# Kernel tuning notes

Measured on AMD Instinct MI355X. Metric: run time of the kernel, lower is better.

The kernel has to match this reference:

```python
import jax, jax.numpy as jnp
import numpy as np

E = 768       # embed dim
NH = 12       # heads
HD = 64       # head dim
WIN = 14      # window size
DEPTH = 12
PATCH = 16
WINDOW_IDX = (0, 1, 3, 4, 6, 7, 9, 10)
EPS = 1e-6


def layer_norm(x, w, b):
    mu = jnp.mean(x, axis=-1, keepdims=True)
    var = jnp.mean(jnp.square(x - mu), axis=-1, keepdims=True)
    return (x - mu) * jax.lax.rsqrt(var + EPS) * w + b


def get_rel_pos(size, rel_pos):
    # q_size == k_size -> direct lookup, no interpolation
    coords = jnp.arange(size)
    rel = coords[:, None] - coords[None, :] + (size - 1)
    return rel_pos[rel]  # (size, size, HD)


def attention(x, qkv_w, qkv_b, proj_w, proj_b, rel_h, rel_w):
    B, H, W, _ = x.shape
    N = H * W
    qkv = (x.reshape(B, N, E) @ qkv_w + qkv_b).reshape(B, N, 3, NH, HD)
    q = qkv[:, :, 0].transpose(0, 2, 1, 3).reshape(B * NH, N, HD)
    k = qkv[:, :, 1].transpose(0, 2, 1, 3).reshape(B * NH, N, HD)
    v = qkv[:, :, 2].transpose(0, 2, 1, 3).reshape(B * NH, N, HD)
    attn = (q * (HD ** -0.5)) @ k.transpose(0, 2, 1)  # (B*NH, N, N)
    # decomposed relative position bias
    Rh = get_rel_pos(H, rel_h)  # (H, H, HD)
    Rw = get_rel_pos(W, rel_w)  # (W, W, HD)
    r_q = q.reshape(B * NH, H, W, HD)
    rh = jnp.einsum('bhwc,hkc->bhwk', r_q, Rh)
    rw = jnp.einsum('bhwc,wkc->bhwk', r_q, Rw)
    attn = attn.reshape(B * NH, H, W, H, W) + rh[:, :, :, :, None] + rw[:, :, :, None, :]
    attn = jax.nn.softmax(attn.reshape(B * NH, N, N), axis=-1)
    out = (attn @ v).reshape(B, NH, H, W, HD).transpose(0, 2, 3, 1, 4).reshape(B, H, W, E)
    return out @ proj_w + proj_b


def window_partition(x, ws):
    B, H, W, C = x.shape
    pad_h, pad_w = (-H) % ws, (-W) % ws
    x = jnp.pad(x, ((0, 0), (0, pad_h), (0, pad_w), (0, 0)))
    Hp, Wp = H + pad_h, W + pad_w
    x = x.reshape(B, Hp // ws, ws, Wp // ws, ws, C).transpose(0, 1, 3, 2, 4, 5)
    return x.reshape(-1, ws, ws, C), (Hp, Wp)


def window_unpartition(win, ws, pad_hw, hw):
    Hp, Wp = pad_hw
    H, W = hw
    B = win.shape[0] // ((Hp // ws) * (Wp // ws))
    x = win.reshape(B, Hp // ws, Wp // ws, ws, ws, -1).transpose(0, 1, 3, 2, 4, 5)
    return x.reshape(B, Hp, Wp, -1)[:, :H, :W]


def _forward(x, patch_w, patch_b, pos_embed,
             ln1_w, ln1_b, qkv_w, qkv_b, proj_w, proj_b,
             rel_h_win, rel_w_win, rel_h_glob, rel_w_glob,
             ln2_w, ln2_b, fc1_w, fc1_b, fc2_w, fc2_b, out_w, out_b):
    # patch embed: conv 16x16 stride 16
    x = jax.lax.conv_general_dilated(
        x, patch_w, (PATCH, PATCH), 'VALID',
        dimension_numbers=('NCHW', 'OIHW', 'NCHW'))
    x = x.transpose(0, 2, 3, 1) + patch_b  # (B, H, W, C)
    x = x + pos_embed
    win_i, glob_i = 0, 0
    for i in range(DEPTH):
        shortcut = x
        h = layer_norm(x, ln1_w[i], ln1_b[i])
        if i in WINDOW_IDX:
            hw = h.shape[1:3]
            h, pad_hw = window_partition(h, WIN)
            h = attention(h, qkv_w[i], qkv_b[i], proj_w[i], proj_b[i],
                          rel_h_win[win_i], rel_w_win[win_i])
            h = window_unpartition(h, WIN, pad_hw, hw)
            win_i += 1
        else:
            h = attention(h, qkv_w[i], qkv_b[i], proj_w[i], proj_b[i],
                          rel_h_glob[glob_i], rel_w_glob[glob_i])
            glob_i += 1
        x = shortcut + h
        h = layer_norm(x, ln2_w[i], ln2_b[i])
        h = jax.nn.gelu(h @ fc1_w[i] + fc1_b[i], approximate=False) @ fc2_w[i] + fc2_b[i]
        x = x + h
    feat = x.transpose(0, 3, 1, 2)  # (B, C, H, W) == 'last_feat'
    return jnp.einsum('bchw,oc->bohw', feat, out_w) + out_b[None, :, None, None]


def setup_inputs() -> dict:
    key = jax.random.key(0)
    ks = iter(jax.random.split(key, 64))
    def n(shape, s=0.02):
        return jax.random.normal(next(ks), shape, jnp.float32) * s
    B, IMG = 2, 512
    G = IMG // PATCH  # 32
    return {
        'x': jax.random.normal(next(ks), (B, 3, IMG, IMG), jnp.float32),
        'patch_w': n((E, 3, PATCH, PATCH)),
        'patch_b': jnp.zeros((E,), jnp.float32),
        'pos_embed': n((1, G, G, E)),
        'ln1_w': jnp.ones((DEPTH, E), jnp.float32),
        'ln1_b': jnp.zeros((DEPTH, E), jnp.float32),
        'qkv_w': n((DEPTH, E, 3 * E)),
        'qkv_b': jnp.zeros((DEPTH, 3 * E), jnp.float32),
        'proj_w': n((DEPTH, E, E)),
        'proj_b': jnp.zeros((DEPTH, E), jnp.float32),
        'rel_h_win': n((8, 2 * WIN - 1, HD)),
        'rel_w_win': n((8, 2 * WIN - 1, HD)),
        'rel_h_glob': n((4, 2 * G - 1, HD)),
        'rel_w_glob': n((4, 2 * G - 1, HD)),
        'ln2_w': jnp.ones((DEPTH, E), jnp.float32),
        'ln2_b': jnp.zeros((DEPTH, E), jnp.float32),
        'fc1_w': n((DEPTH, E, 4 * E)),
        'fc1_b': jnp.zeros((DEPTH, 4 * E), jnp.float32),
        'fc2_w': n((DEPTH, 4 * E, E)),
        'fc2_b': jnp.zeros((DEPTH, E), jnp.float32),
        'out_w': n((256, E)),
        'out_b': jnp.zeros((256,), jnp.float32),
    }


def reference(x, patch_w, patch_b, pos_embed,
              ln1_w, ln1_b, qkv_w, qkv_b, proj_w, proj_b,
              rel_h_win, rel_w_win, rel_h_glob, rel_w_glob,
              ln2_w, ln2_b, fc1_w, fc1_b, fc2_w, fc2_b, out_w, out_b):
    return _forward(x, patch_w, patch_b, pos_embed,
                    ln1_w, ln1_b, qkv_w, qkv_b, proj_w, proj_b,
                    rel_h_win, rel_w_win, rel_h_glob, rel_w_glob,
                    ln2_w, ln2_b, fc1_w, fc1_b, fc2_w, fc2_b, out_w, out_b)
```

## Files before the change

### kernel.cpp

```cpp
#include <hip/hip_runtime.h>
#include <hip/hip_bf16.h>
#include <math.h>

static constexpr int E   = 768;
static constexpr int NH  = 12;
static constexpr int HD  = 64;
static constexpr int Bsz = 2;
static constexpr int G   = 32;
static constexpr int NTOK = G * G;
static constexpr int ROWS = Bsz * NTOK;
static constexpr int WS  = 14;
static constexpr int NWIN_SIDE = 3;
static constexpr int NWIN = NWIN_SIDE * NWIN_SIDE;
static constexpr int BW  = Bsz * NWIN;
static constexpr int NW  = WS * WS;
static constexpr int WROWS = BW * NW;
static constexpr int WIN_MASK = 0x6DB;

typedef __attribute__((ext_vector_type(8))) short short8;
typedef __attribute__((ext_vector_type(4))) float f32x4;
typedef unsigned short ushort_t;

__device__ __forceinline__ unsigned short f2bf(float x) {
  union { float f; unsigned u; } v; v.f = x;
  unsigned r = v.u + 0x7fffu + ((v.u >> 16) & 1u);
  return (unsigned short)(r >> 16);
}
__device__ __forceinline__ float bf2f(unsigned short h) {
  union { unsigned u; float f; } v; v.u = ((unsigned)h) << 16;
  return v.f;
}

__device__ __forceinline__ void glds16(const void* g, void* l) {
  __builtin_amdgcn_global_load_lds(
      (const __attribute__((address_space(1))) unsigned*)g,
      (__attribute__((address_space(3))) unsigned*)l, 16, 0, 0);
}

__global__ __launch_bounds__(256) void ln_kernel(
    const float* __restrict__ in, const float* __restrict__ w,
    const float* __restrict__ b, ushort_t* __restrict__ out) {
  const int wave = threadIdx.x >> 6, lane = threadIdx.x & 63;
  const int row = blockIdx.x * 4 + wave;
  const float4* r4 = (const float4*)(in + (size_t)row * E);
  float4 v[3];
  v[0] = r4[lane]; v[1] = r4[lane + 64]; v[2] = r4[lane + 128];
  float s = 0.f, s2 = 0.f;
#pragma unroll
  for (int i = 0; i < 3; i++) {
    s += v[i].x + v[i].y + v[i].z + v[i].w;
    s2 += v[i].x * v[i].x + v[i].y * v[i].y + v[i].z * v[i].z + v[i].w * v[i].w;
  }
#pragma unroll
  for (int off = 1; off <= 32; off <<= 1) {
    s += __shfl_xor(s, off);
    s2 += __shfl_xor(s2, off);
  }
  const float mean = s * (1.f / E);
  const float var  = s2 * (1.f / E) - mean * mean;
  const float rs   = rsqrtf(var + 1e-6f);
  ushort_t* o = out + (size_t)row * E;
#pragma unroll
  for (int i = 0; i < 3; i++) {
    const int e0 = (lane + i * 64) * 4;
    ushort4 p;
    p.x = f2bf((v[i].x - mean) * rs * w[e0]     + b[e0]);
    p.y = f2bf((v[i].y - mean) * rs * w[e0 + 1] + b[e0 + 1]);
    p.z = f2bf((v[i].z - mean) * rs * w[e0 + 2] + b[e0 + 2]);
    p.w = f2bf((v[i].w - mean) * rs * w[e0 + 3] + b[e0 + 3]);
    *(ushort4*)&o[e0] = p;
  }
}

enum { OP_QKV = 0, OP_GELU = 1, OP_ADD = 2, OP_POS = 3, OP_HEAD = 4 };

template <int OP, int MAP>
__global__ __launch_bounds__(256) void gemm_bt(
    const ushort_t* __restrict__ A, const ushort_t* __restrict__ Bt,
    const float* __restrict__ bias, const float* __restrict__ res,
    const float* __restrict__ pos, void* __restrict__ Cp,
    int M, int N, int K, int ncol) {
  __shared__ ushort_t As[2][64 * 64];
  __shared__ ushort_t Bs[2][64 * 64];
  const int tid = threadIdx.x, wave = tid >> 6, lane = tid & 63;
  const int lx = lane & 15, ly = lane >> 4;

  const int nwg = gridDim.x;
  const int q = nwg >> 3, r = nwg & 7;
  const int xcd = blockIdx.x & 7, loc = blockIdx.x >> 3;
  const int wgid = ((xcd < r) ? xcd * (q + 1) : r * (q + 1) + (xcd - r) * q) + loc;
  const int brow = wgid / ncol, bcol = wgid - brow * ncol;
  const int row0 = brow * 64, col0 = bcol * 64;
  const int wm = (wave >> 1) * 32, wn = (wave & 1) * 32;
  const int rin = lane >> 3, pseg = lane & 7;
  const int lseg = pseg ^ rin;
  f32x4 acc[2][2] = {};

  const ushort_t* aptr[2];
  const ushort_t* bptr[2];
#pragma unroll
  for (int j = 0; j < 2; j++) {
    const int slot = wave * 2 + j;
    int ar = row0 + slot * 8 + rin;
    if (ar >= M) ar = M - 1;
    if (MAP == 2) {
      const int bI = ar >> 10, t = ar & 1023, y = t >> 5, x = t & 31;
      const int by = y / WS, wy = y - by * WS;
      const int bx = x / WS, wx = x - bx * WS;
      const int win = bI * NWIN + by * NWIN_SIDE + bx;
      aptr[j] = &A[((size_t)win * NW + wy * WS + wx) * E + lseg * 8];
    } else {
      aptr[j] = &A[(size_t)ar * K + lseg * 8];
    }
    const int br = col0 + slot * 8 + rin;
    bptr[j] = &Bt[(size_t)br * K + lseg * 8];
  }

#pragma unroll
  for (int j = 0; j < 2; j++) {
    const int slot = wave * 2 + j;
    glds16(aptr[j], &As[0][slot * 512]);
    glds16(bptr[j], &Bs[0][slot * 512]);
  }

  const int nt = K >> 6;
  for (int t = 0; t < nt; t++) {
    const int cur = t & 1;
    if (t + 1 < nt) {
      const int k1 = (t + 1) << 6;
#pragma unroll
      for (int j = 0; j < 2; j++) {
        const int slot = wave * 2 + j;
        glds16(aptr[j] + k1, &As[cur ^ 1][slot * 512]);
        glds16(bptr[j] + k1, &Bs[cur ^ 1][slot * 512]);
      }
      asm volatile("s_waitcnt vmcnt(4)" ::: "memory");
    } else {
      asm volatile("s_waitcnt vmcnt(0)" ::: "memory");
    }
    __builtin_amdgcn_s_barrier();
    __builtin_amdgcn_sched_barrier(0);
#pragma unroll
    for (int kb = 0; kb < 2; kb++) {
      short8 af[2], bfm[2];
#pragma unroll
      for (int m = 0; m < 2; m++) {
        const int rr = wm + m * 16 + lx;
        af[m] = *(const short8*)&As[cur][rr * 64 + (((kb * 4 + ly) ^ (rr & 7)) * 8)];
      }
#pragma unroll
      for (int n = 0; n < 2; n++) {
        const int rr = wn + n * 16 + lx;
        bfm[n] = *(const short8*)&Bs[cur][rr * 64 + (((kb * 4 + ly) ^ (rr & 7)) * 8)];
      }
      __builtin_amdgcn_s_setprio(1);
#pragma unroll
      for (int m = 0; m < 2; m++)
#pragma unroll
        for (int n = 0; n < 2; n++)
          acc[m][n] = __builtin_amdgcn_mfma_f32_16x16x32_bf16(af[m], bfm[n], acc[m][n], 0, 0, 0);
      __builtin_amdgcn_s_setprio(0);
    }
    asm volatile("s_waitcnt lgkmcnt(0)" ::: "memory");
    __builtin_amdgcn_s_barrier();
    __builtin_amdgcn_sched_barrier(0);
  }

#pragma unroll
  for (int m = 0; m < 2; m++) {
#pragma unroll
    for (int r4 = 0; r4 < 4; r4++) {
      const int gr = row0 + wm + m * 16 + ly * 4 + r4;
      if (gr >= M) continue;
#pragma unroll
      for (int n = 0; n < 2; n++) {
        const int gc = col0 + wn + n * 16 + lx;
        float v = acc[m][n][r4] + bias[gc];
        if (OP == OP_GELU) v = 0.5f * v * (1.f + erff(v * 0.70710678118654752f));
        if (OP == OP_ADD)  v += res[(size_t)gr * N + gc];
        if (OP == OP_POS)  v += pos[(size_t)(gr & 1023) * N + gc];
        if (OP == OP_QKV || OP == OP_GELU)
          ((ushort_t*)Cp)[(size_t)gr * N + gc] = f2bf(v);
        else if (OP == OP_HEAD)
          ((float*)Cp)[(((size_t)(gr >> 10) * 256 + gc) << 10) | (gr & 1023)] = v;
        else
          ((float*)Cp)[(size_t)gr * N + gc] = v;
      }
    }
  }
}

template <int OP, int MAP>
__global__ __launch_bounds__(128) void gemm_32(
    const ushort_t* __restrict__ A, const ushort_t* __restrict__ Bt,
    const float* __restrict__ bias, const float* __restrict__ res,
    const float* __restrict__ pos, void* __restrict__ Cp,
    int M, int N, int K, int ncol) {
  __shared__ ushort_t As[2][32 * 64];
  __shared__ ushort_t Bs[2][64 * 64];
  const int tid = threadIdx.x, wave = tid >> 6, lane = tid & 63;
  const int lx = lane & 15, ly = lane >> 4;

  const int nwg = gridDim.x;
  const int q = nwg >> 3, r = nwg & 7;
  const int xcd = blockIdx.x & 7, loc = blockIdx.x >> 3;
  const int wgid = ((xcd < r) ? xcd * (q + 1) : r * (q + 1) + (xcd - r) * q) + loc;
  const int brow = wgid / ncol, bcol = wgid - brow * ncol;
  const int row0 = brow * 32, col0 = bcol * 64;
  const int wn = wave * 32;
  const int rin = lane >> 3, pseg = lane & 7;
  const int lseg = pseg ^ rin;
  f32x4 acc[2][2] = {};

  const ushort_t* aptr[2];
  const ushort_t* bptr[4];
#pragma unroll
  for (int j = 0; j < 2; j++) {
    const int slot = wave * 2 + j;
    int ar = row0 + slot * 8 + rin;
    if (ar >= M) ar = M - 1;
    if (MAP == 2) {
      const int bI = ar >> 10, t = ar & 1023, y = t >> 5, x = t & 31;
      const int by = y / WS, wy = y - by * WS;
      const int bx = x / WS, wx = x - bx * WS;
      const int win = bI * NWIN + by * NWIN_SIDE + bx;
      aptr[j] = &A[((size_t)win * NW + wy * WS + wx) * E + lseg * 8];
    } else {
      aptr[j] = &A[(size_t)ar * K + lseg * 8];
    }
  }
#pragma unroll
  for (int j = 0; j < 4; j++) {
    const int slot = wave * 4 + j;
    const int br = col0 + slot * 8 + rin;
    bptr[j] = &Bt[(size_t)br * K + lseg * 8];
  }

#pragma unroll
  for (int j = 0; j < 2; j++) glds16(aptr[j], &As[0][(wave * 2 + j) * 512]);
#pragma unroll
  for (int j = 0; j < 4; j++) glds16(bptr[j], &Bs[0][(wave * 4 + j) * 512]);

  const int nt = K >> 6;
  for (int t = 0; t < nt; t++) {
    const int cur = t & 1;
    if (t + 1 < nt) {
      const int k1 = (t + 1) << 6;
#pragma unroll
      for (int j = 0; j < 2; j++) glds16(aptr[j] + k1, &As[cur ^ 1][(wave * 2 + j) * 512]);
#pragma unroll
      for (int j = 0; j < 4; j++) glds16(bptr[j] + k1, &Bs[cur ^ 1][(wave * 4 + j) * 512]);
      asm volatile("s_waitcnt vmcnt(6)" ::: "memory");
    } else {
      asm volatile("s_waitcnt vmcnt(0)" ::: "memory");
    }
    __builtin_amdgcn_s_barrier();
    __builtin_amdgcn_sched_barrier(0);
#pragma unroll
    for (int kb = 0; kb < 2; kb++) {
      short8 af[2], bfm[2];
#pragma unroll
      for (int m = 0; m < 2; m++) {
        const int rr = m * 16 + lx;
        af[m] = *(const short8*)&As[cur][rr * 64 + (((kb * 4 + ly) ^ (rr & 7)) * 8)];
      }
#pragma unroll
      for (int n = 0; n < 2; n++) {
        const int rr = wn + n * 16 + lx;
        bfm[n] = *(const short8*)&Bs[cur][rr * 64 + (((kb * 4 + ly) ^ (rr & 7)) * 8)];
      }
      __builtin_amdgcn_s_setprio(1);
#pragma unroll
      for (int m = 0; m < 2; m++)
#pragma unroll
        for (int n = 0; n < 2; n++)
          acc[m][n] = __builtin_amdgcn_mfma_f32_16x16x32_bf16(af[m], bfm[n], acc[m][n], 0, 0, 0);
      __builtin_amdgcn_s_setprio(0);
    }
    asm volatile("s_waitcnt lgkmcnt(0)" ::: "memory");
    __builtin_amdgcn_s_barrier();
    __builtin_amdgcn_sched_barrier(0);
  }

#pragma unroll
  for (int m = 0; m < 2; m++) {
#pragma unroll
    for (int r4 = 0; r4 < 4; r4++) {
      const int gr = row0 + m * 16 + ly * 4 + r4;
      if (gr >= M) continue;
#pragma unroll
      for (int n = 0; n < 2; n++) {
        const int gc = col0 + wn + n * 16 + lx;
        float v = acc[m][n][r4] + bias[gc];
        if (OP == OP_GELU) v = 0.5f * v * (1.f + erff(v * 0.70710678118654752f));
        if (OP == OP_ADD)  v += res[(size_t)gr * N + gc];
        if (OP == OP_POS)  v += pos[(size_t)(gr & 1023) * N + gc];
        if (OP == OP_QKV || OP == OP_GELU)
          ((ushort_t*)Cp)[(size_t)gr * N + gc] = f2bf(v);
        else if (OP == OP_HEAD)
          ((float*)Cp)[(((size_t)(gr >> 10) * 256 + gc) << 10) | (gr & 1023)] = v;
        else
          ((float*)Cp)[(size_t)gr * N + gc] = v;
      }
    }
  }
}

__global__ __launch_bounds__(128) void attn_mfma(
    const ushort_t* __restrict__ qkv, ushort_t* __restrict__ out,
    const float* __restrict__ relh, const float* __restrict__ relw,
    int Hd, int Wd) {
  const int Ntok = Hd * Wd;
  __shared__ ushort_t smem[11392];
  ushort_t* Ks   = smem;
  ushort_t* Vst  = smem + 2048;
  ushort_t* Ps   = smem + 4608;
  ushort_t* Qs   = smem;
  ushort_t* RelS = smem + 2048;
  ushort_t* Th   = smem + 6144;
  ushort_t* Tw   = smem + 8256;
  ushort_t* khw  = smem + 10368;

  const int tid = threadIdx.x, wave = tid >> 6, lane = tid & 63;
  const int lx = lane & 15, ly = lane >> 4;
  const int bh = blockIdx.y, b = bh / NH, nh = bh % NH;
  const int q0 = blockIdx.x * 32;
  const size_t base = (size_t)b * Ntok * 2304 + nh * 64;

#pragma unroll
  for (int i = 0; i < 2; i++) {
    const int fv = i * 128 + tid;
    const int row = fv >> 3, dv8 = (fv & 7) * 8;
    const int qq = min(q0 + row, Ntok - 1);
    short8 v = *(const short8*)&qkv[base + (size_t)qq * 2304 + dv8];
    *(short8*)&Qs[(row * 64 + dv8) ^ ((row & 7) << 3)] = v;
  }
  for (int k = tid; k < 1024; k += 128) {
    const int kc = min(k, Ntok - 1);
    const int kh = kc / Wd;
    khw[k] = (ushort_t)((kh << 8) | (kc - kh * Wd));
  }
  __syncthreads();

  short8 qa[2];
  {
    const int row = wave * 16 + lx;
#pragma unroll
    for (int kb = 0; kb < 2; kb++)
      qa[kb] = *(const short8*)&Qs[(row * 64 + kb * 32 + ly * 8) ^ ((row & 7) << 3)];
  }
  int qh_r[4], qw_r[4];
#pragma unroll
  for (int r = 0; r < 4; r++) {
    const int qc = min(q0 + wave * 16 + ly * 4 + r, Ntok - 1);
    qh_r[r] = qc / Wd;
    qw_r[r] = qc - qh_r[r] * Wd;
  }

  for (int t = 0; t < 2; t++) {
    const float* rel = t ? relw : relh;
    const int TR = t ? (2 * Wd - 1) : (2 * Hd - 1);
    __syncthreads();
#pragma unroll
    for (int i = 0; i < 4; i++) {
      const int fv = i * 128 + tid;
      const int row = fv >> 3, c8 = (fv & 7) * 8;
      short8 v = {};
      if (row < TR) {
        const float* rp = &rel[(size_t)row * 64 + c8];
        const float4 a = *(const float4*)rp;
        const float4 bq = *(const float4*)(rp + 4);
        v[0] = (short)f2bf(a.x);  v[1] = (short)f2bf(a.y);
        v[2] = (short)f2bf(a.z);  v[3] = (short)f2bf(a.w);
        v[4] = (short)f2bf(bq.x); v[5] = (short)f2bf(bq.y);
        v[6] = (short)f2bf(bq.z); v[7] = (short)f2bf(bq.w);
      }
      *(short8*)&RelS[(row * 64 + c8) ^ ((row & 7) << 3)] = v;
    }
    __syncthreads();
    const int NT = (TR + 15) >> 4;
    ushort_t* T = t ? Tw : Th;
    for (int nt = 0; nt < NT; nt++) {
      f32x4 a = {};
      __builtin_amdgcn_s_setprio(1);
#pragma unroll
      for (int kb = 0; kb < 2; kb++) {
        const int rrow = nt * 16 + lx;
        short8 bfv = *(const short8*)&RelS[(rrow * 64 + kb * 32 + ly * 8) ^ ((rrow & 7) << 3)];
        a = __builtin_amdgcn_mfma_f32_16x16x32_bf16(qa[kb], bfv, a, 0, 0, 0);
      }
      __builtin_amdgcn_s_setprio(0);
#pragma unroll
      for (int reg = 0; reg < 4; reg++)
        T[(wave * 16 + ly * 4 + reg) * 66 + nt * 16 + lx] = f2bf(a[reg]);
    }
  }

  f32x4 o[4] = {};
  float m_[4], l_[4];
#pragma unroll
  for (int r = 0; r < 4; r++) { m_[r] = -3e38f; l_[r] = 0.f; }

  const int nkt = (Ntok + 31) >> 5;
  const int srow = tid >> 3, c7 = tid & 7, dv8s = c7 * 8;
  const int vswz = (c7 & 3) << 3;

  short8 kpre[2], vpre[2];
#pragma unroll
  for (int i = 0; i < 2; i++) {
    const int gk = srow + i * 16;
    short8 kv = {}, vv = {};
    if (gk < Ntok) {
      kv = *(const short8*)&qkv[base + 768 + (size_t)gk * 2304 + dv8s];
      vv = *(const short8*)&qkv[base + 1536 + (size_t)gk * 2304 + dv8s];
    }
    kpre[i] = kv; vpre[i] = vv;
  }

  for (int kt = 0; kt < nkt; kt++) {
    __syncthreads();
#pragma unroll
    for (int i = 0; i < 2; i++) {
      const int row = srow + i * 16;
      *(short8*)&Ks[(row * 64 + dv8s) ^ ((row & 7) << 3)] = kpre[i];
      const int kcol = row ^ vswz;
#pragma unroll
      for (int j = 0; j < 8; j++)
        Vst[(dv8s + j) * 40 + kcol] = (ushort_t)vpre[i][j];
    }
    if (kt + 1 < nkt) {
#pragma unroll
      for (int i = 0; i < 2; i++) {
        const int gk = (kt + 1) * 32 + srow + i * 16;
        short8 kv = {}, vv = {};
        if (gk < Ntok) {
          kv = *(const short8*)&qkv[base + 768 + (size_t)gk * 2304 + dv8s];
          vv = *(const short8*)&qkv[base + 1536 + (size_t)gk * 2304 + dv8s];
        }
        kpre[i] = kv; vpre[i] = vv;
      }
    }
    __syncthreads();

    f32x4 c[2] = {};
    __builtin_amdgcn_s_setprio(1);
#pragma unroll
    for (int kb = 0; kb < 2; kb++)
#pragma unroll
      for (int ct = 0; ct < 2; ct++) {
        const int krow = ct * 16 + lx;
        short8 kf = *(const short8*)&Ks[(krow * 64 + kb * 32 + ly * 8) ^ ((krow & 7) << 3)];
        c[ct] = __builtin_amdgcn_mfma_f32_16x16x32_bf16(qa[kb], kf, c[ct], 0, 0, 0);
      }
    __builtin_amdgcn_s_setprio(0);

    const int k0a = kt * 32 + lx, k1a = k0a + 16;
    const int tv0 = khw[k0a], tv1 = khw[k1a];
    const int kh0 = tv0 >> 8, kw0 = tv0 & 255;
    const int kh1 = tv1 >> 8, kw1 = tv1 & 255;
    float pv0[4], pv1[4], mt[4];
#pragma unroll
    for (int r = 0; r < 4; r++) {
      const int trow = (wave * 16 + ly * 4 + r) * 66;
      float s0 = c[0][r] * 0.125f + bf2f(Th[trow + qh_r[r] - kh0 + Hd - 1])
               + bf2f(Tw[trow + qw_r[r] - kw0 + Wd - 1]);
      float s1 = c[1][r] * 0.125f + bf2f(Th[trow + qh_r[r] - kh1 + Hd - 1])
               + bf2f(Tw[trow + qw_r[r] - kw1 + Wd - 1]);
      if (k0a >= Ntok) s0 = -1e30f;
      if (k1a >= Ntok) s1 = -1e30f;
      pv0[r] = s0; pv1[r] = s1;
      mt[r] = fmaxf(s0, s1);
    }
    const float dmax = fmaxf(fmaxf(mt[0] - m_[0], mt[1] - m_[1]),
                             fmaxf(mt[2] - m_[2], mt[3] - m_[3]));
    if (!__all(dmax <= 8.f)) {
#pragma unroll
      for (int r = 0; r < 4; r++) {
        float mr = mt[r];
#pragma unroll
        for (int off = 1; off <= 8; off <<= 1) mr = fmaxf(mr, __shfl_xor(mr, off));
        const float mn = fmaxf(m_[r], mr);
        const float sc = __expf(m_[r] - mn);
        m_[r] = mn; l_[r] *= sc;
#pragma unroll
        for (int dt = 0; dt < 4; dt++) o[dt][r] *= sc;
      }
    }
#pragma unroll
    for (int r = 0; r < 4; r++) {
      const float p0 = __expf(pv0[r] - m_[r]);
      const float p1 = __expf(pv1[r] - m_[r]);
      l_[r] += p0 + p1;
      const int pb = wave * 640 + (ly * 4 + r) * 40;
      Ps[pb + lx]      = f2bf(p0);
      Ps[pb + 16 + lx] = f2bf(p1);
    }
    short8 pf = *(const short8*)&Ps[wave * 640 + lx * 40 + ly * 8];
    __builtin_amdgcn_s_setprio(1);
#pragma unroll
    for (int dt = 0; dt < 4; dt++) {
      const int drow = dt * 16 + lx;
      short8 vf = *(const short8*)&Vst[drow * 40 + ((ly * 8) ^ (((drow >> 3) & 3) << 3))];
      o[dt] = __builtin_amdgcn_mfma_f32_16x16x32_bf16(pf, vf, o[dt], 0, 0, 0);
    }
    __builtin_amdgcn_s_setprio(0);
  }

#pragma unroll
  for (int r = 0; r < 4; r++) {
#pragma unroll
    for (int off = 1; off <= 8; off <<= 1) l_[r] += __shfl_xor(l_[r], off);
    const int qq = q0 + wave * 16 + ly * 4 + r;
    if (qq >= Ntok) continue;
    const float inv = 1.f / l_[r];
#pragma unroll
    for (int dt = 0; dt < 4; dt++)
      out[((size_t)b * Ntok + qq) * E + nh * 64 + dt * 16 + lx] = f2bf(o[dt][r] * inv);
  }
}

__global__ __launch_bounds__(128) void qkv_winpart(
    const ushort_t* __restrict__ qi, const float* __restrict__ qkvb,
    ushort_t* __restrict__ qw) {
  const int row = blockIdx.x;
  const int win = row / NW, t = row - win * NW;
  const int wy = t / WS, wx = t - wy * WS;
  const int b = win / NWIN, wr = win - b * NWIN;
  const int by = wr / NWIN_SIDE, bx = wr - by * NWIN_SIDE;
  const int y = by * WS + wy, x = bx * WS + wx;
  short8* dst = (short8*)(qw + (size_t)row * 2304);
  if (y < G && x < G) {
    const short8* src = (const short8*)(qi + (((size_t)b * G + y) * G + x) * 2304);
    for (int e = threadIdx.x; e < 288; e += 128) dst[e] = src[e];
  } else {
    for (int e = threadIdx.x; e < 288; e += 128) {
      short8 v;
#pragma unroll
      for (int j = 0; j < 8; j++) v[j] = (short)f2bf(qkvb[e * 8 + j]);
      dst[e] = v;
    }
  }
}

__global__ __launch_bounds__(256) void im2col(const float* __restrict__ x,
                                              ushort_t* __restrict__ out) {
  const int blk = blockIdx.x;
  const int b = blk >> 10, t = blk & 1023, gy = t >> 5, gx = t & 31;
  for (int k = threadIdx.x; k < 768; k += 256) {
    const int ci = k >> 8, rem = k & 255, py = rem >> 4, px = rem & 15;
    out[(size_t)blk * 768 + k] =
        f2bf(x[(((size_t)b * 3 + ci) * 512 + gy * 16 + py) * 512 + gx * 16 + px]);
  }
}

__global__ __launch_bounds__(256) void prep_wt64(
    const float* __restrict__ qkvw, const float* __restrict__ projw,
    const float* __restrict__ fc1w, const float* __restrict__ fc2w,
    ushort_t* __restrict__ wq, ushort_t* __restrict__ wp,
    ushort_t* __restrict__ w1, ushort_t* __restrict__ w2) {
  __shared__ float tile[64][65];
  const int blk = blockIdx.x;
  const float* W; ushort_t* Wt; int Kd, Nd, tn, tk;
  if (blk < 432)       { W = qkvw;  Wt = wq; Kd = 768;  Nd = 2304; tn = blk % 36;          tk = blk / 36; }
  else if (blk < 576)  { W = projw; Wt = wp; Kd = 768;  Nd = 768;  tn = (blk - 432) % 12;  tk = (blk - 432) / 12; }
  else if (blk < 1152) { W = fc1w;  Wt = w1; Kd = 768;  Nd = 3072; tn = (blk - 576) % 48;  tk = (blk - 576) / 48; }
  else                 { W = fc2w;  Wt = w2; Kd = 3072; Nd = 768;  tn = (blk - 1152) % 12; tk = (blk - 1152) / 12; }
  const int k0 = tk * 64, n0 = tn * 64;
  const int kr = threadIdx.x >> 2, cg = (threadIdx.x & 3) * 16;
  const float* src = &W[(size_t)(k0 + kr) * Nd + n0 + cg];
#pragma unroll
  for (int j = 0; j < 4; j++) {
    const float4 v = *(const float4*)&src[j * 4];
    tile[kr][cg + j * 4 + 0] = v.x;
    tile[kr][cg + j * 4 + 1] = v.y;
    tile[kr][cg + j * 4 + 2] = v.z;
    tile[kr][cg + j * 4 + 3] = v.w;
  }
  __syncthreads();
  const int nr = kr;
  short8 o0, o1;
#pragma unroll
  for (int j = 0; j < 8; j++) o0[j] = (short)f2bf(tile[cg + j][nr]);
#pragma unroll
  for (int j = 0; j < 8; j++) o1[j] = (short)f2bf(tile[cg + 8 + j][nr]);
  ushort_t* dst = &Wt[(size_t)(n0 + nr) * Kd + k0 + cg];
  *(short8*)&dst[0] = o0;
  *(short8*)&dst[8] = o1;
}

__global__ __launch_bounds__(256) void cast_bf16(const float* __restrict__ in,
                                                 ushort_t* __restrict__ out, int n) {
  const int idx = (blockIdx.x * 256 + threadIdx.x) * 4;
  if (idx + 3 < n) {
    const float4 v = *(const float4*)&in[idx];
    ushort4 p;
    p.x = f2bf(v.x); p.y = f2bf(v.y); p.z = f2bf(v.z); p.w = f2bf(v.w);
    *(ushort4*)&out[idx] = p;
  }
}

extern "C" void kernel_launch(void* const* d_in, const int* in_sizes, int n_in,
                              void* d_out, int out_size, void* d_ws, size_t ws_size,
                              hipStream_t stream) {
  const float* x_in     = (const float*)d_in[0];
  const float* patch_w  = (const float*)d_in[1];
  const float* patch_b  = (const float*)d_in[2];
  const float* pos_emb  = (const float*)d_in[3];
  const float* ln1_w    = (const float*)d_in[4];
  const float* ln1_b    = (const float*)d_in[5];
  const float* qkv_w    = (const float*)d_in[6];
  const float* qkv_b    = (const float*)d_in[7];
  const float* proj_w   = (const float*)d_in[8];
  const float* proj_b   = (const float*)d_in[9];
  const float* rel_h_w  = (const float*)d_in[10];
  const float* rel_w_w  = (const float*)d_in[11];
  const float* rel_h_g  = (const float*)d_in[12];
  const float* rel_w_g  = (const float*)d_in[13];
  const float* ln2_w    = (const float*)d_in[14];
  const float* ln2_b    = (const float*)d_in[15];
  const float* fc1_w    = (const float*)d_in[16];
  const float* fc1_b    = (const float*)d_in[17];
  const float* fc2_w    = (const float*)d_in[18];
  const float* fc2_b    = (const float*)d_in[19];
  const float* out_w    = (const float*)d_in[20];
  const float* out_b    = (const float*)d_in[21];
  float* outp = (float*)d_out;

  float* xbuf = (float*)d_ws;
  ushort_t* hb16    = (ushort_t*)(xbuf + (size_t)ROWS * E);
  ushort_t* qkvimg  = hb16 + (size_t)ROWS * E;
  ushort_t* qkvwin  = qkvimg + (size_t)ROWS * 3 * E;
  ushort_t* attnw16 = qkvwin + (size_t)WROWS * 3 * E;
  ushort_t* h1b16   = attnw16 + (size_t)WROWS * E;
  ushort_t* wq      = h1b16 + (size_t)ROWS * 4 * E;
  ushort_t* wp      = wq + (size_t)2304 * 768;
  ushort_t* w1      = wp + (size_t)768 * 768;
  ushort_t* w2      = w1 + (size_t)3072 * 768;
  ushort_t* pwT16   = w2 + (size_t)768 * 3072;
  ushort_t* headW16 = pwT16 + (size_t)768 * 768;
  ushort_t* imb16 = hb16;

  cast_bf16<<<576, 256, 0, stream>>>(patch_w, pwT16, 768 * 768);
  cast_bf16<<<192, 256, 0, stream>>>(out_w, headW16, 256 * 768);

  im2col<<<ROWS, 256, 0, stream>>>(x_in, imb16);
  gemm_32<OP_POS, 0><<<768, 128, 0, stream>>>(
      imb16, pwT16, patch_b, nullptr, pos_emb, xbuf, ROWS, E, E, 12);

  int win_i = 0, glob_i = 0;
  for (int i = 0; i < 12; i++) {
    const bool is_win = (WIN_MASK >> i) & 1;

    prep_wt64<<<1728, 256, 0, stream>>>(
        qkv_w + (size_t)i * E * 3 * E, proj_w + (size_t)i * E * E,
        fc1_w + (size_t)i * E * 4 * E, fc2_w + (size_t)i * 4 * E * E,
        wq, wp, w1, w2);

    ln_kernel<<<ROWS / 4, 256, 0, stream>>>(xbuf, ln1_w + i * E, ln1_b + i * E, hb16);

    gemm_bt<OP_QKV, 0><<<36 * 32, 256, 0, stream>>>(
        hb16, wq, qkv_b + i * 3 * E, nullptr, nullptr, qkvimg, ROWS, 3 * E, E, 36);

    if (is_win) {
      qkv_winpart<<<WROWS, 128, 0, stream>>>(qkvimg, qkv_b + i * 3 * E, qkvwin);
      attn_mfma<<<dim3(7, BW * NH), 128, 0, stream>>>(
          qkvwin, attnw16, rel_h_w + (size_t)win_i * (2 * WS - 1) * HD,
          rel_w_w + (size_t)win_i * (2 * WS - 1) * HD, WS, WS);
      win_i++;
      gemm_32<OP_ADD, 2><<<768, 128, 0, stream>>>(
          attnw16, wp, proj_b + i * E, xbuf, nullptr, xbuf, ROWS, E, E, 12);
    } else {
      attn_mfma<<<dim3(32, Bsz * NH), 128, 0, stream>>>(
          qkvimg, attnw16, rel_h_g + (size_t)glob_i * (2 * G - 1) * HD,
          rel_w_g + (size_t)glob_i * (2 * G - 1) * HD, G, G);
      glob_i++;
      gemm_32<OP_ADD, 0><<<768, 128, 0, stream>>>(
          attnw16, wp, proj_b + i * E, xbuf, nullptr, xbuf, ROWS, E, E, 12);
    }

    ln_kernel<<<ROWS / 4, 256, 0, stream>>>(xbuf, ln2_w + i * E, ln2_b + i * E, hb16);
    gemm_bt<OP_GELU, 0><<<48 * 32, 256, 0, stream>>>(
        hb16, w1, fc1_b + i * 4 * E, nullptr, nullptr, h1b16, ROWS, 4 * E, E, 48);
    gemm_32<OP_ADD, 0><<<768, 128, 0, stream>>>(
        h1b16, w2, fc2_b + i * E, xbuf, nullptr, xbuf, ROWS, E, 4 * E, 12);
  }

  cast_bf16<<<1536, 256, 0, stream>>>(xbuf, hb16, ROWS * E);
  gemm_32<OP_HEAD, 0><<<256, 128, 0, stream>>>(
      hb16, headW16, out_b, nullptr, nullptr, outp, ROWS, 256, E, 4);
}
```

Baseline: 1.807 ms.

## Fuse window partition into attention and use 64-query blocks with 256 threads

Removes the separate qkv_winpart kernel and its copy buffer. The attention kernel now gathers window rows directly from the image-layout QKV through a per-block row index table, and substitutes the bias for padded tokens. Each block now handles 64 queries with 4 waves instead of 32 with 2, halving redundant K/V loads and rel-pos table setup per query. This uses more shared memory and fewer, larger blocks, which may reduce occupancy and grid parallelism, especially in the windowed layers.

```diff
diff --git a/kernel.cpp b/kernel.cpp
--- a/kernel.cpp
+++ b/kernel.cpp
@@ -306,39 +306,63 @@
   }
 }
 
-__global__ __launch_bounds__(128) void attn_mfma(
+template <int WIN>
+__global__ __launch_bounds__(256) void attn64(
     const ushort_t* __restrict__ qkv, ushort_t* __restrict__ out,
     const float* __restrict__ relh, const float* __restrict__ relw,
-    int Hd, int Wd) {
+    const float* __restrict__ qkvb, int Hd, int Wd) {
   const int Ntok = Hd * Wd;
-  __shared__ ushort_t smem[11392];
+  __shared__ ushort_t smem[17664];
   ushort_t* Ks   = smem;
   ushort_t* Vst  = smem + 2048;
+  ushort_t* Qs   = smem;
+  ushort_t* RelS = smem;
   ushort_t* Ps   = smem + 4608;
-  ushort_t* Qs   = smem;
-  ushort_t* RelS = smem + 2048;
-  ushort_t* Th   = smem + 6144;
-  ushort_t* Tw   = smem + 8256;
-  ushort_t* khw  = smem + 10368;
+  ushort_t* Th   = smem + 7168;
+  ushort_t* Tw   = smem + 11392;
+  ushort_t* khw  = smem + 15616;
+  ushort_t* ridx = smem + 16640;
 
   const int tid = threadIdx.x, wave = tid >> 6, lane = tid & 63;
   const int lx = lane & 15, ly = lane >> 4;
-  const int bh = blockIdx.y, b = bh / NH, nh = bh % NH;
-  const int q0 = blockIdx.x * 32;
-  const size_t base = (size_t)b * Ntok * 2304 + nh * 64;
+  const int bh = blockIdx.y;
+  const int nh = bh % NH, wb = bh / NH;
+  int by = 0, bx = 0, b_img;
+  if (WIN) {
+    b_img = wb / NWIN;
+    const int wr = wb - b_img * NWIN;
+    by = wr / NWIN_SIDE; bx = wr - by * NWIN_SIDE;
+  } else {
+    b_img = wb;
+  }
+  const int q0 = blockIdx.x * 64;
+  const size_t base = (size_t)b_img * NTOK * 2304 + nh * 64;
+
+  for (int k = tid; k < 1024; k += 256) {
+    const int kc = min(k, Ntok - 1);
+    const int kh = kc / Wd, kw = kc - kh * Wd;
+    khw[k] = (ushort_t)((kh << 8) | kw);
+    if (WIN) {
+      const int gy = by * WS + kh, gx = bx * WS + kw;
+      ridx[k] = (gy < G && gx < G) ? (ushort_t)(gy * G + gx) : (ushort_t)0xFFFF;
+    }
+  }
+  __syncthreads();
 
 #pragma unroll
   for (int i = 0; i < 2; i++) {
-    const int fv = i * 128 + tid;
+    const int fv = i * 256 + tid;
     const int row = fv >> 3, dv8 = (fv & 7) * 8;
     const int qq = min(q0 + row, Ntok - 1);
-    short8 v = *(const short8*)&qkv[base + (size_t)qq * 2304 + dv8];
+    int rI;
+    if (WIN) {
+      const int t = ridx[qq];
+      rI = (t == 0xFFFF) ? 0 : t;
+    } else {
+      rI = qq;
+    }
+    short8 v = *(const short8*)&qkv[base + (size_t)rI * 2304 + dv8];
     *(short8*)&Qs[(row * 64 + dv8) ^ ((row & 7) << 3)] = v;
-  }
-  for (int k = tid; k < 1024; k += 128) {
-    const int kc = min(k, Ntok - 1);
-    const int kh = kc / Wd;
-    khw[k] = (ushort_t)((kh << 8) | (kc - kh * Wd));
   }
   __syncthreads();
 
@@ -356,14 +380,14 @@
     qh_r[r] = qc / Wd;
     qw_r[r] = qc - qh_r[r] * Wd;
   }
+  __syncthreads();
 
   for (int t = 0; t < 2; t++) {
     const float* rel = t ? relw : relh;
     const int TR = t ? (2 * Wd - 1) : (2 * Hd - 1);
-    __syncthreads();
-#pragma unroll
-    for (int i = 0; i < 4; i++) {
-      const int fv = i * 128 + tid;
+#pragma unroll
+    for (int i = 0; i < 2; i++) {
+      const int fv = i * 256 + tid;
       const int row = fv >> 3, c8 = (fv & 7) * 8;
       short8 v = {};
       if (row < TR) {
@@ -394,6 +418,7 @@
       for (int reg = 0; reg < 4; reg++)
         T[(wave * 16 + ly * 4 + reg) * 66 + nt * 16 + lx] = f2bf(a[reg]);
     }
+    __syncthreads();
   }
 
   f32x4 o[4] = {};
@@ -405,41 +430,47 @@
   const int srow = tid >> 3, c7 = tid & 7, dv8s = c7 * 8;
   const int vswz = (c7 & 3) << 3;
 
-  short8 kpre[2], vpre[2];
-#pragma unroll
-  for (int i = 0; i < 2; i++) {
-    const int gk = srow + i * 16;
-    short8 kv = {}, vv = {};
+  short8 kb8 = {}, vb8 = {};
+  if (WIN) {
+#pragma unroll
+    for (int j = 0; j < 8; j++) {
+      kb8[j] = (short)f2bf(qkvb[768 + nh * 64 + dv8s + j]);
+      vb8[j] = (short)f2bf(qkvb[1536 + nh * 64 + dv8s + j]);
+    }
+  }
+
+  auto load_kv = [&](int gk, short8& kv, short8& vv) {
+    kv = short8{}; vv = short8{};
     if (gk < Ntok) {
-      kv = *(const short8*)&qkv[base + 768 + (size_t)gk * 2304 + dv8s];
-      vv = *(const short8*)&qkv[base + 1536 + (size_t)gk * 2304 + dv8s];
-    }
-    kpre[i] = kv; vpre[i] = vv;
-  }
+      if (WIN) {
+        const int rI = ridx[gk];
+        if (rI != 0xFFFF) {
+          const size_t a = base + (size_t)rI * 2304;
+          kv = *(const short8*)&qkv[a + 768 + dv8s];
+          vv = *(const short8*)&qkv[a + 1536 + dv8s];
+        } else { kv = kb8; vv = vb8; }
+      } else {
+        const size_t a = base + (size_t)gk * 2304;
+        kv = *(const short8*)&qkv[a + 768 + dv8s];
+        vv = *(const short8*)&qkv[a + 1536 + dv8s];
+      }
+    }
+  };
+
+  short8 kpre, vpre;
+  load_kv(srow, kpre, vpre);
 
   for (int kt = 0; kt < nkt; kt++) {
     __syncthreads();
-#pragma unroll
-    for (int i = 0; i < 2; i++) {
-      const int row = srow + i * 16;
-      *(short8*)&Ks[(row * 64 + dv8s) ^ ((row & 7) << 3)] = kpre[i];
+    {
+      const int row = srow;
+      *(short8*)&Ks[(row * 64 + dv8s) ^ ((row & 7) << 3)] = kpre;
       const int kcol = row ^ vswz;
 #pragma unroll
       for (int j = 0; j < 8; j++)
-        Vst[(dv8s + j) * 40 + kcol] = (ushort_t)vpre[i][j];
-    }
-    if (kt + 1 < nkt) {
-#pragma unroll
-      for (int i = 0; i < 2; i++) {
-        const int gk = (kt + 1) * 32 + srow + i * 16;
-        short8 kv = {}, vv = {};
-        if (gk < Ntok) {
-          kv = *(const short8*)&qkv[base + 768 + (size_t)gk * 2304 + dv8s];
-          vv = *(const short8*)&qkv[base + 1536 + (size_t)gk * 2304 + dv8s];
-        }
-        kpre[i] = kv; vpre[i] = vv;
-      }
-    }
+        Vst[(dv8s + j) * 40 + kcol] = (ushort_t)vpre[j];
+    }
+    if (kt + 1 < nkt) load_kv((kt + 1) * 32 + srow, kpre, vpre);
     __syncthreads();
 
     f32x4 c[2] = {};
@@ -455,7 +486,7 @@
     __builtin_amdgcn_s_setprio(0);
 
     const int k0a = kt * 32 + lx, k1a = k0a + 16;
-    const int tv0 = khw[k0a], tv1 = khw[k1a];
+    const int tv0 = khw[min(k0a, 1023)], tv1 = khw[min(k1a, 1023)];
     const int kh0 = tv0 >> 8, kw0 = tv0 & 255;
     const int kh1 = tv1 >> 8, kw1 = tv1 & 255;
     float pv0[4], pv1[4], mt[4];
@@ -512,33 +543,11 @@
     for (int off = 1; off <= 8; off <<= 1) l_[r] += __shfl_xor(l_[r], off);
     const int qq = q0 + wave * 16 + ly * 4 + r;
     if (qq >= Ntok) continue;
+    const size_t orow = WIN ? ((size_t)wb * NW + qq) : ((size_t)b_img * NTOK + qq);
     const float inv = 1.f / l_[r];
 #pragma unroll
     for (int dt = 0; dt < 4; dt++)
-      out[((size_t)b * Ntok + qq) * E + nh * 64 + dt * 16 + lx] = f2bf(o[dt][r] * inv);
-  }
-}
-
-__global__ __launch_bounds__(128) void qkv_winpart(
-    const ushort_t* __restrict__ qi, const float* __restrict__ qkvb,
-    ushort_t* __restrict__ qw) {
-  const int row = blockIdx.x;
-  const int win = row / NW, t = row - win * NW;
-  const int wy = t / WS, wx = t - wy * WS;
-  const int b = win / NWIN, wr = win - b * NWIN;
-  const int by = wr / NWIN_SIDE, bx = wr - by * NWIN_SIDE;
-  const int y = by * WS + wy, x = bx * WS + wx;
-  short8* dst = (short8*)(qw + (size_t)row * 2304);
-  if (y < G && x < G) {
-    const short8* src = (const short8*)(qi + (((size_t)b * G + y) * G + x) * 2304);
-    for (int e = threadIdx.x; e < 288; e += 128) dst[e] = src[e];
-  } else {
-    for (int e = threadIdx.x; e < 288; e += 128) {
-      short8 v;
-#pragma unroll
-      for (int j = 0; j < 8; j++) v[j] = (short)f2bf(qkvb[e * 8 + j]);
-      dst[e] = v;
-    }
+      out[orow * E + nh * 64 + dt * 16 + lx] = f2bf(o[dt][r] * inv);
   }
 }
 
@@ -629,8 +638,7 @@
   float* xbuf = (float*)d_ws;
   ushort_t* hb16    = (ushort_t*)(xbuf + (size_t)ROWS * E);
   ushort_t* qkvimg  = hb16 + (size_t)ROWS * E;
-  ushort_t* qkvwin  = qkvimg + (size_t)ROWS * 3 * E;
-  ushort_t* attnw16 = qkvwin + (size_t)WROWS * 3 * E;
+  ushort_t* attnw16 = qkvimg + (size_t)ROWS * 3 * E;
   ushort_t* h1b16   = attnw16 + (size_t)WROWS * E;
   ushort_t* wq      = h1b16 + (size_t)ROWS * 4 * E;
   ushort_t* wp      = wq + (size_t)2304 * 768;
@@ -662,17 +670,16 @@
         hb16, wq, qkv_b + i * 3 * E, nullptr, nullptr, qkvimg, ROWS, 3 * E, E, 36);
 
     if (is_win) {
-      qkv_winpart<<<WROWS, 128, 0, stream>>>(qkvimg, qkv_b + i * 3 * E, qkvwin);
-      attn_mfma<<<dim3(7, BW * NH), 128, 0, stream>>>(
-          qkvwin, attnw16, rel_h_w + (size_t)win_i * (2 * WS - 1) * HD,
-          rel_w_w + (size_t)win_i * (2 * WS - 1) * HD, WS, WS);
+      attn64<1><<<dim3(4, BW * NH), 256, 0, stream>>>(
+          qkvimg, attnw16, rel_h_w + (size_t)win_i * (2 * WS - 1) * HD,
+          rel_w_w + (size_t)win_i * (2 * WS - 1) * HD, qkv_b + i * 3 * E, WS, WS);
       win_i++;
       gemm_32<OP_ADD, 2><<<768, 128, 0, stream>>>(
           attnw16, wp, proj_b + i * E, xbuf, nullptr, xbuf, ROWS, E, E, 12);
     } else {
-      attn_mfma<<<dim3(32, Bsz * NH), 128, 0, stream>>>(
+      attn64<0><<<dim3(16, Bsz * NH), 256, 0, stream>>>(
           qkvimg, attnw16, rel_h_g + (size_t)glob_i * (2 * G - 1) * HD,
-          rel_w_g + (size_t)glob_i * (2 * G - 1) * HD, G, G);
+          rel_w_g + (size_t)glob_i * (2 * G - 1) * HD, qkv_b + i * 3 * E, G, G);
       glob_i++;
       gemm_32<OP_ADD, 0><<<768, 128, 0, stream>>>(
           attnw16, wp, proj_b + i * E, xbuf, nullptr, xbuf, ROWS, E, E, 12);
```

Measured after the change: 1.719 ms (median of 2 runs). 1.05x faster.
